# Kernel tuning notes

Hardware: AMD Instinct MI355X
Metric: run time of the kernel (lower is better)

## Reference

```python
import jax, jax.numpy as jnp
import numpy as np

CHANNELS = 32


def _mlp(x, W1, b1, W2, b2, W3, b3):
    # FNN: Linear -> ReLU -> Linear -> ReLU -> Linear (last layer linear)
    h = jax.nn.relu(x @ W1 + b1)
    h = jax.nn.relu(h @ W2 + b2)
    return h @ W3 + b3


def setup_inputs() -> dict:
    key = jax.random.key(0)
    ks = jax.random.split(key, 8)
    E = 262144
    C = CHANNELS
    H = 128
    d_in = 4  # 2 * spatial_dim
    d_out = C * (C + 1)  # 1056
    s = lambda fan_in: 1.0 / np.sqrt(fan_in)
    return {
        "pos_i": jax.random.normal(ks[0], (E, 2), jnp.float32),
        "pos_j": jax.random.normal(ks[1], (E, 2), jnp.float32),
        "v_j": jax.random.normal(ks[2], (E, C), jnp.float32),
        "W1": jax.random.normal(ks[3], (d_in, H), jnp.float32) * s(d_in),
        "b1": jnp.zeros((H,), jnp.float32),
        "W2": jax.random.normal(ks[4], (H, H), jnp.float32) * s(H),
        "b2": jnp.zeros((H,), jnp.float32),
        "W3": jax.random.normal(ks[5], (H, d_out), jnp.float32) * s(H),
        "b3": jnp.zeros((d_out,), jnp.float32),
    }


def reference(pos_i, pos_j, v_j, W1, b1, W2, b2, W3, b3):
    C = CHANNELS
    pos_ij = jnp.concatenate((pos_i, pos_j), axis=-1)          # [E, 2*spatial_dim]
    kernel = _mlp(pos_ij, W1, b1, W2, b2, W3, b3)
    kernel = kernel.reshape(-1, C, C + 1)                      # [E, C, C+1]
    mat, bias = kernel[..., :, :-1], kernel[..., :, -1]        # [E,C,C], [E,C]
    return jnp.einsum('eij,ej->ei', mat, v_j) + bias           # [E, C]
```

## Files before the change

kernel.cpp:

```cpp
#include <hip/hip_runtime.h>


#define E_TOTAL 262144
#define EPB 256
#define NBLK (E_TOTAL / EPB)

typedef float f32x4 __attribute__((ext_vector_type(4)));
typedef short s8v  __attribute__((ext_vector_type(8)));

__device__ __forceinline__ unsigned short f2bf(float x) {
  unsigned u = __float_as_uint(x);
  u += 0x7fffu + ((u >> 16) & 1u);
  return (unsigned short)(u >> 16);
}

__global__ void prep_pack(const float* __restrict__ W2, const float* __restrict__ W3,
                          const float* __restrict__ b3,
                          unsigned short* __restrict__ Wg2, unsigned short* __restrict__ W2f,
                          unsigned short* __restrict__ b3f, float* __restrict__ b3c) {
  int idx = blockIdx.x * 256 + threadIdx.x;
  if (idx < 135168) {
    int jj = idx & 7, lane = (idx >> 3) & 63;
    int ksnn = idx >> 9, ks = ksnn & 3, nn = ksnn >> 2;
    int nnt = (nn < 33) ? (2 * nn) : (2 * (nn - 33) + 1);
    int k = ks * 32 + ((lane >> 4) << 3) + jj;
    int col = nnt * 16 + (lane & 15);
    int i = col & 31, j = col >> 5;
    Wg2[idx] = f2bf(W3[k * 1056 + i * 33 + j]);
  }
  if (idx < 16384) {
    int ks = idx >> 12, nt = (idx >> 9) & 7, l = (idx >> 3) & 63, jj = idx & 7;
    int k = ks * 32 + ((l >> 4) << 3) + jj;
    int n = nt * 16 + (l & 15);
    W2f[idx] = f2bf(W2[k * 128 + n]);
  }
  if (idx < 1024) {
    int jj = idx & 7, lane = (idx >> 3) & 63, ih = idx >> 9;
    int j = ((lane >> 4) << 3) + jj, i = ih * 16 + (lane & 15);
    b3f[idx] = f2bf(b3[i * 33 + j]);
  }
  if (idx < 32) b3c[idx] = b3[idx * 33 + 32];
}

__device__ __forceinline__ void tile_load(s8v (&dst)[4], const unsigned short* __restrict__ Wg2,
                                          int n, int lane) {
  const s8v* src = (const s8v*)(Wg2 + (size_t)n * 2048 + lane * 8);
#pragma unroll
  for (int ks = 0; ks < 4; ++ks) dst[ks] = src[ks * 64];
}

template <int IH>
__device__ __forceinline__ void tile_compute(const s8v (&bf)[4], const float* __restrict__ vt,
                                             int j, int eoff,
                                             const s8v (&af)[4][4], float (&oa)[2][4][4]) {
  const f32x4 zero4 = {0.f, 0.f, 0.f, 0.f};
  const float* vp = vt + j * 260 + eoff;
#pragma unroll
  for (int m = 0; m < 4; ++m) {
    f32x4 p = __builtin_amdgcn_mfma_f32_16x16x32_bf16(af[m][0], bf[0], zero4, 0, 0, 0);
#pragma unroll
    for (int ks = 1; ks < 4; ++ks)
      p = __builtin_amdgcn_mfma_f32_16x16x32_bf16(af[m][ks], bf[ks], p, 0, 0, 0);
    f32x4 vv = *(const f32x4*)(vp + m * 16);
#pragma unroll
    for (int r = 0; r < 4; ++r) oa[IH][m][r] += vv[r] * p[r];
  }
}

__global__ __launch_bounds__(256, 2) void fnn_fused(
    const float* __restrict__ pos_i, const float* __restrict__ pos_j,
    const float* __restrict__ vj, const float* __restrict__ W1,
    const float* __restrict__ b1, const float* __restrict__ b2,
    const unsigned short* __restrict__ W2f, const unsigned short* __restrict__ Wg2,
    const unsigned short* __restrict__ b3f, const float* __restrict__ b3c,
    float* __restrict__ out) {
  __shared__ __attribute__((aligned(16))) char smem[34320];
  float* vt = (float*)smem;
  unsigned short* h2n = (unsigned short*)smem;
  unsigned short* h1c = (unsigned short*)(smem + 17408);

  const int tid = threadIdx.x;
  const int w = tid >> 6, lane = tid & 63, q = lane >> 4, ln = lane & 15;
  const int B0 = blockIdx.x * EPB;
  const int eoff = w * 64 + q * 4;

  float oa[2][4][4];
  {
    s8v av[4];
#pragma unroll
    for (int m = 0; m < 4; ++m) {
      int e = B0 + w * 64 + m * 16 + ln;
      const float4 va = *(const float4*)(vj + (size_t)e * 32 + q * 8);
      const float4 vb = *(const float4*)(vj + (size_t)e * 32 + q * 8 + 4);
      s8v t;
      t[0] = (short)f2bf(va.x); t[1] = (short)f2bf(va.y);
      t[2] = (short)f2bf(va.z); t[3] = (short)f2bf(va.w);
      t[4] = (short)f2bf(vb.x); t[5] = (short)f2bf(vb.y);
      t[6] = (short)f2bf(vb.z); t[7] = (short)f2bf(vb.w);
      av[m] = t;
    }
#pragma unroll
    for (int ih = 0; ih < 2; ++ih) {
      s8v b3fr = *(const s8v*)(b3f + (ih * 64 + lane) * 8);
      float cbv = b3c[ih * 16 + ln];
      f32x4 ci = {cbv, cbv, cbv, cbv};
#pragma unroll
      for (int m = 0; m < 4; ++m) {
        f32x4 p = __builtin_amdgcn_mfma_f32_16x16x32_bf16(av[m], b3fr, ci, 0, 0, 0);
#pragma unroll
        for (int r = 0; r < 4; ++r) oa[ih][m][r] = p[r];
      }
    }
  }

  const int hh0 = (tid & 15) * 8;
  float w1r[4][8], b1r[8];
#pragma unroll
  for (int d = 0; d < 4; ++d)
#pragma unroll
    for (int u = 0; u < 8; ++u) w1r[d][u] = W1[d * 128 + hh0 + u];
#pragma unroll
  for (int u = 0; u < 8; ++u) b1r[u] = b1[hh0 + u];

  s8v af[4][4];
  for (int qtr = 0; qtr < 4; ++qtr) {
    for (int cb = 0; cb < 2; ++cb) {
#pragma unroll
      for (int half = 0; half < 2; ++half) {
        int ee = (tid >> 4) + half * 16;
        int eg = B0 + qtr * 64 + cb * 32 + ee;
        float2 pi = *(const float2*)(pos_i + (size_t)eg * 2);
        float2 pj = *(const float2*)(pos_j + (size_t)eg * 2);
        s8v hv;
#pragma unroll
        for (int u = 0; u < 8; ++u) {
          float o = b1r[u] + pi.x * w1r[0][u] + pi.y * w1r[1][u] +
                    pj.x * w1r[2][u] + pj.y * w1r[3][u];
          hv[u] = (short)f2bf(fmaxf(o, 0.f));
        }
        *(s8v*)&h1c[ee * 136 + hh0] = hv;
      }
      __syncthreads();
#pragma unroll
      for (int s = 0; s < 4; ++s) {
        int tt = w * 4 + s, mt = tt >> 3, nt = tt & 7;
        f32x4 a4 = {0.f, 0.f, 0.f, 0.f};
#pragma unroll
        for (int ks = 0; ks < 4; ++ks) {
          s8v afr = *(const s8v*)&h1c[(mt * 16 + ln) * 136 + ks * 32 + q * 8];
          s8v bfr = *(const s8v*)(W2f + ((ks * 8 + nt) * 64 + lane) * 8);
          a4 = __builtin_amdgcn_mfma_f32_16x16x32_bf16(afr, bfr, a4, 0, 0, 0);
        }
        float b2v = b2[nt * 16 + ln];
        int eb = cb * 32 + mt * 16 + q * 4;
        int kc = nt * 16 + ln;
#pragma unroll
        for (int r = 0; r < 4; ++r)
          h2n[(eb + r) * 136 + kc] = f2bf(fmaxf(a4[r] + b2v, 0.f));
      }
      __syncthreads();
    }
    if (w == qtr) {
#pragma unroll
      for (int m = 0; m < 4; ++m)
#pragma unroll
        for (int ks = 0; ks < 4; ++ks)
          af[m][ks] = *(const s8v*)&h2n[(m * 16 + ln) * 136 + ks * 32 + q * 8];
    }
    __syncthreads();
  }

  s8v bf[4];
  tile_load(bf, Wg2, 0, lane);

  {
    const float* vrow = vj + (size_t)(B0 + tid) * 32;
#pragma unroll
    for (int j4 = 0; j4 < 8; ++j4) {
      float4 vv = *(const float4*)(vrow + j4 * 4);
      vt[(j4 * 4 + 0) * 260 + tid] = vv.x;
      vt[(j4 * 4 + 1) * 260 + tid] = vv.y;
      vt[(j4 * 4 + 2) * 260 + tid] = vv.z;
      vt[(j4 * 4 + 3) * 260 + tid] = vv.w;
    }
    vt[32 * 260 + tid] = 1.0f;
  }

#pragma unroll 1
  for (int n = 0; n < 33; ++n) {
    tile_compute<0>(bf, vt, n, eoff, af, oa);
    tile_load(bf, Wg2, n + 1, lane);
  }
#pragma unroll 1
  for (int n = 33; n < 66; ++n) {
    tile_compute<1>(bf, vt, n - 33, eoff, af, oa);
    tile_load(bf, Wg2, n + 1, lane);
  }

#pragma unroll
  for (int m = 0; m < 4; ++m)
#pragma unroll
    for (int ih = 0; ih < 2; ++ih)
#pragma unroll
      for (int r = 0; r < 4; ++r) {
        int e = B0 + w * 64 + m * 16 + q * 4 + r;
        out[(size_t)e * 32 + ih * 16 + ln] = oa[ih][m][r];
      }
}

extern "C" void kernel_launch(void* const* d_in, const int* in_sizes, int n_in,
                              void* d_out, int out_size, void* d_ws, size_t ws_size,
                              hipStream_t stream) {
  const float* pos_i = (const float*)d_in[0];
  const float* pos_j = (const float*)d_in[1];
  const float* vj    = (const float*)d_in[2];
  const float* W1    = (const float*)d_in[3];
  const float* b1    = (const float*)d_in[4];
  const float* W2    = (const float*)d_in[5];
  const float* b2    = (const float*)d_in[6];
  const float* W3    = (const float*)d_in[7];
  const float* b3    = (const float*)d_in[8];
  float* outp = (float*)d_out;

  unsigned short* Wg2 = (unsigned short*)d_ws;
  unsigned short* W2f = (unsigned short*)((char*)d_ws + 270336);
  unsigned short* b3f = (unsigned short*)((char*)d_ws + 303104);
  float*          b3c = (float*)((char*)d_ws + 305152);

  prep_pack<<<528, 256, 0, stream>>>(W2, W3, b3, Wg2, W2f, b3f, b3c);
  fnn_fused<<<NBLK, 256, 0, stream>>>(pos_i, pos_j, vj, W1, b1, b2, W2f, Wg2, b3f, b3c, outp);
}
```

Before: 184.8 us.

## Double-buffer W3 tile loads and split output halves to cut accumulator registers

The W3 tile loop now uses two register buffers so each global load has a full tile of compute to hide behind, instead of being consumed right after issue. The accumulator array shrinks from two output halves to one: the first half is stored and the second half re-initialised from v_j and the b3 bias between the two loops. This frees registers for the extra buffer, at the cost of re-reading v_j and earlier-issued stores. The v_j load for the FMA is also moved ahead of the MFMA chain.

```diff
diff --git a/kernel.cpp b/kernel.cpp
--- a/kernel.cpp
+++ b/kernel.cpp
@@ -49,22 +49,55 @@
   for (int ks = 0; ks < 4; ++ks) dst[ks] = src[ks * 64];
 }
 
-template <int IH>
 __device__ __forceinline__ void tile_compute(const s8v (&bf)[4], const float* __restrict__ vt,
                                              int j, int eoff,
-                                             const s8v (&af)[4][4], float (&oa)[2][4][4]) {
+                                             const s8v (&af)[4][4], float (&oa)[4][4]) {
   const f32x4 zero4 = {0.f, 0.f, 0.f, 0.f};
   const float* vp = vt + j * 260 + eoff;
 #pragma unroll
   for (int m = 0; m < 4; ++m) {
+    f32x4 vv = *(const f32x4*)(vp + m * 16);
     f32x4 p = __builtin_amdgcn_mfma_f32_16x16x32_bf16(af[m][0], bf[0], zero4, 0, 0, 0);
 #pragma unroll
     for (int ks = 1; ks < 4; ++ks)
       p = __builtin_amdgcn_mfma_f32_16x16x32_bf16(af[m][ks], bf[ks], p, 0, 0, 0);
-    f32x4 vv = *(const f32x4*)(vp + m * 16);
-#pragma unroll
-    for (int r = 0; r < 4; ++r) oa[IH][m][r] += vv[r] * p[r];
-  }
+#pragma unroll
+    for (int r = 0; r < 4; ++r) oa[m][r] += vv[r] * p[r];
+  }
+}
+
+__device__ __forceinline__ void init_oa(float (&oa)[4][4], const float* __restrict__ vj,
+                                        const unsigned short* __restrict__ b3f,
+                                        const float* __restrict__ b3c,
+                                        int B0, int w, int q, int ln, int lane, int ih) {
+  s8v b3fr = *(const s8v*)(b3f + (ih * 64 + lane) * 8);
+  float cbv = b3c[ih * 16 + ln];
+  f32x4 ci = {cbv, cbv, cbv, cbv};
+#pragma unroll
+  for (int m = 0; m < 4; ++m) {
+    int e = B0 + w * 64 + m * 16 + ln;
+    const float4 va = *(const float4*)(vj + (size_t)e * 32 + q * 8);
+    const float4 vb = *(const float4*)(vj + (size_t)e * 32 + q * 8 + 4);
+    s8v t;
+    t[0] = (short)f2bf(va.x); t[1] = (short)f2bf(va.y);
+    t[2] = (short)f2bf(va.z); t[3] = (short)f2bf(va.w);
+    t[4] = (short)f2bf(vb.x); t[5] = (short)f2bf(vb.y);
+    t[6] = (short)f2bf(vb.z); t[7] = (short)f2bf(vb.w);
+    f32x4 p = __builtin_amdgcn_mfma_f32_16x16x32_bf16(t, b3fr, ci, 0, 0, 0);
+#pragma unroll
+    for (int r = 0; r < 4; ++r) oa[m][r] = p[r];
+  }
+}
+
+__device__ __forceinline__ void store_half(float* __restrict__ out, const float (&oa)[4][4],
+                                           int B0, int w, int q, int ln, int ih) {
+#pragma unroll
+  for (int m = 0; m < 4; ++m)
+#pragma unroll
+    for (int r = 0; r < 4; ++r) {
+      int e = B0 + w * 64 + m * 16 + q * 4 + r;
+      out[(size_t)e * 32 + ih * 16 + ln] = oa[m][r];
+    }
 }
 
 __global__ __launch_bounds__(256, 2) void fnn_fused(
@@ -84,34 +117,8 @@
   const int B0 = blockIdx.x * EPB;
   const int eoff = w * 64 + q * 4;
 
-  float oa[2][4][4];
-  {
-    s8v av[4];
-#pragma unroll
-    for (int m = 0; m < 4; ++m) {
-      int e = B0 + w * 64 + m * 16 + ln;
-      const float4 va = *(const float4*)(vj + (size_t)e * 32 + q * 8);
-      const float4 vb = *(const float4*)(vj + (size_t)e * 32 + q * 8 + 4);
-      s8v t;
-      t[0] = (short)f2bf(va.x); t[1] = (short)f2bf(va.y);
-      t[2] = (short)f2bf(va.z); t[3] = (short)f2bf(va.w);
-      t[4] = (short)f2bf(vb.x); t[5] = (short)f2bf(vb.y);
-      t[6] = (short)f2bf(vb.z); t[7] = (short)f2bf(vb.w);
-      av[m] = t;
-    }
-#pragma unroll
-    for (int ih = 0; ih < 2; ++ih) {
-      s8v b3fr = *(const s8v*)(b3f + (ih * 64 + lane) * 8);
-      float cbv = b3c[ih * 16 + ln];
-      f32x4 ci = {cbv, cbv, cbv, cbv};
-#pragma unroll
-      for (int m = 0; m < 4; ++m) {
-        f32x4 p = __builtin_amdgcn_mfma_f32_16x16x32_bf16(av[m], b3fr, ci, 0, 0, 0);
-#pragma unroll
-        for (int r = 0; r < 4; ++r) oa[ih][m][r] = p[r];
-      }
-    }
-  }
+  float oa[4][4];
+  init_oa(oa, vj, b3f, b3c, B0, w, q, ln, lane, 0);
 
   const int hh0 = (tid & 15) * 8;
   float w1r[4][8], b1r[8];
@@ -170,8 +177,9 @@
     __syncthreads();
   }
 
-  s8v bf[4];
-  tile_load(bf, Wg2, 0, lane);
+  s8v bfA[4], bfB[4];
+  tile_load(bfA, Wg2, 0, lane);
+  tile_load(bfB, Wg2, 1, lane);
 
   {
     const float* vrow = vj + (size_t)(B0 + tid) * 32;
@@ -187,25 +195,27 @@
   }
 
 #pragma unroll 1
-  for (int n = 0; n < 33; ++n) {
-    tile_compute<0>(bf, vt, n, eoff, af, oa);
-    tile_load(bf, Wg2, n + 1, lane);
-  }
+  for (int c = 0; c < 16; ++c) {
+    tile_compute(bfA, vt, 2 * c,     eoff, af, oa);
+    tile_load(bfA, Wg2, 2 * c + 2, lane);
+    tile_compute(bfB, vt, 2 * c + 1, eoff, af, oa);
+    tile_load(bfB, Wg2, 2 * c + 3, lane);
+  }
+  tile_compute(bfA, vt, 32, eoff, af, oa);
+  tile_load(bfA, Wg2, 34, lane);
+
+  store_half(out, oa, B0, w, q, ln, 0);
+  init_oa(oa, vj, b3f, b3c, B0, w, q, ln, lane, 1);
+
 #pragma unroll 1
-  for (int n = 33; n < 66; ++n) {
-    tile_compute<1>(bf, vt, n - 33, eoff, af, oa);
-    tile_load(bf, Wg2, n + 1, lane);
-  }
-
-#pragma unroll
-  for (int m = 0; m < 4; ++m)
-#pragma unroll
-    for (int ih = 0; ih < 2; ++ih)
-#pragma unroll
-      for (int r = 0; r < 4; ++r) {
-        int e = B0 + w * 64 + m * 16 + q * 4 + r;
-        out[(size_t)e * 32 + ih * 16 + ln] = oa[ih][m][r];
-      }
+  for (int c = 0; c < 16; ++c) {
+    tile_compute(bfB, vt, 2 * c,     eoff, af, oa);
+    tile_load(bfB, Wg2, 35 + 2 * c, lane);
+    tile_compute(bfA, vt, 2 * c + 1, eoff, af, oa);
+    tile_load(bfA, Wg2, 36 + 2 * c, lane);
+  }
+  tile_compute(bfB, vt, 32, eoff, af, oa);
+  store_half(out, oa, B0, w, q, ln, 1);
 }
 
 extern "C" void kernel_launch(void* const* d_in, const int* in_sizes, int n_in,
```

New measurement: 184.9 us. Within noise of the previous version (+0.1%).

## Stage W2 fragments in LDS and restructure layer-2 into 64-edge chunks

Applied to the files above, without the earlier changes.

Copies the packed W2 bf16 fragments into shared memory with direct global-to-LDS loads at kernel start, so layer-2 MFMA operands are read from LDS instead of global memory on every chunk. Layer 2 now handles 64 edges per step, each wave computing 16 rows across all 8 column tiles. This halves the barriers per quarter and removes one, and b2 is hoisted into registers. The prep kernel is rewritten to read W3/W2 coalesced and scatter writes. LDS use roughly doubles to about 66KB, which may limit occupancy to two blocks per CU and must still fit with launch bounds.

```diff
diff --git a/kernel.cpp b/kernel.cpp
--- a/kernel.cpp
+++ b/kernel.cpp
@@ -7,11 +7,17 @@
 
 typedef float f32x4 __attribute__((ext_vector_type(4)));
 typedef short s8v  __attribute__((ext_vector_type(8)));
+typedef unsigned int u32;
 
 __device__ __forceinline__ unsigned short f2bf(float x) {
   unsigned u = __float_as_uint(x);
   u += 0x7fffu + ((u >> 16) & 1u);
   return (unsigned short)(u >> 16);
+}
+
+__device__ __forceinline__ void ld16_g2l(const void* g, void* l) {
+  __builtin_amdgcn_global_load_lds((const __attribute__((address_space(1))) u32*)g,
+                                   (__attribute__((address_space(3))) u32*)l, 16, 0, 0);
 }
 
 __global__ void prep_pack(const float* __restrict__ W2, const float* __restrict__ W3,
@@ -20,19 +26,23 @@
                           unsigned short* __restrict__ b3f, float* __restrict__ b3c) {
   int idx = blockIdx.x * 256 + threadIdx.x;
   if (idx < 135168) {
-    int jj = idx & 7, lane = (idx >> 3) & 63;
-    int ksnn = idx >> 9, ks = ksnn & 3, nn = ksnn >> 2;
-    int nnt = (nn < 33) ? (2 * nn) : (2 * (nn - 33) + 1);
-    int k = ks * 32 + ((lane >> 4) << 3) + jj;
-    int col = nnt * 16 + (lane & 15);
-    int i = col & 31, j = col >> 5;
-    Wg2[idx] = f2bf(W3[k * 1056 + i * 33 + j]);
+    int k = idx / 1056, c = idx % 1056;
+    int i = c / 33, jc = c % 33;
+    int col = jc * 32 + i;
+    int nnt = col >> 4, low = col & 15;
+    int nn = (nnt & 1) ? (33 + (nnt >> 1)) : (nnt >> 1);
+    int ks = k >> 5, kr = k & 31;
+    int lane = ((kr >> 3) << 4) + low;
+    int jj = k & 7;
+    Wg2[((nn * 4 + ks) * 64 + lane) * 8 + jj] = f2bf(W3[idx]);
   }
   if (idx < 16384) {
-    int ks = idx >> 12, nt = (idx >> 9) & 7, l = (idx >> 3) & 63, jj = idx & 7;
-    int k = ks * 32 + ((l >> 4) << 3) + jj;
-    int n = nt * 16 + (l & 15);
-    W2f[idx] = f2bf(W2[k * 128 + n]);
+    int k = idx >> 7, n = idx & 127;
+    int ks = k >> 5, kr = k & 31;
+    int nt = n >> 4, low = n & 15;
+    int l = ((kr >> 3) << 4) + low;
+    int jj = k & 7;
+    W2f[((ks * 8 + nt) * 64 + l) * 8 + jj] = f2bf(W2[idx]);
   }
   if (idx < 1024) {
     int jj = idx & 7, lane = (idx >> 3) & 63, ih = idx >> 9;
@@ -74,15 +84,24 @@
     const unsigned short* __restrict__ W2f, const unsigned short* __restrict__ Wg2,
     const unsigned short* __restrict__ b3f, const float* __restrict__ b3c,
     float* __restrict__ out) {
-  __shared__ __attribute__((aligned(16))) char smem[34320];
+  __shared__ __attribute__((aligned(16))) char smem[67584];
   float* vt = (float*)smem;
-  unsigned short* h2n = (unsigned short*)smem;
-  unsigned short* h1c = (unsigned short*)(smem + 17408);
+  unsigned short* h1c = (unsigned short*)smem;
+  unsigned short* h2n = (unsigned short*)(smem + 17408);
+  unsigned short* W2L = (unsigned short*)(smem + 34816);
 
   const int tid = threadIdx.x;
   const int w = tid >> 6, lane = tid & 63, q = lane >> 4, ln = lane & 15;
   const int B0 = blockIdx.x * EPB;
   const int eoff = w * 64 + q * 4;
+
+  {
+    const unsigned short* src = W2f + tid * 8;
+    char* dstb = smem + 34816 + w * 1024;
+#pragma unroll
+    for (int cc = 0; cc < 8; ++cc)
+      ld16_g2l(src + cc * 2048, dstb + cc * 4096);
+  }
 
   float oa[2][4][4];
   {
@@ -114,52 +133,52 @@
   }
 
   const int hh0 = (tid & 15) * 8;
-  float w1r[4][8], b1r[8];
+  float w1r[4][8], b1r[8], b2r[8];
 #pragma unroll
   for (int d = 0; d < 4; ++d)
 #pragma unroll
     for (int u = 0; u < 8; ++u) w1r[d][u] = W1[d * 128 + hh0 + u];
 #pragma unroll
   for (int u = 0; u < 8; ++u) b1r[u] = b1[hh0 + u];
+#pragma unroll
+  for (int s = 0; s < 8; ++s) b2r[s] = b2[s * 16 + ln];
 
   s8v af[4][4];
   for (int qtr = 0; qtr < 4; ++qtr) {
-    for (int cb = 0; cb < 2; ++cb) {
-#pragma unroll
-      for (int half = 0; half < 2; ++half) {
-        int ee = (tid >> 4) + half * 16;
-        int eg = B0 + qtr * 64 + cb * 32 + ee;
-        float2 pi = *(const float2*)(pos_i + (size_t)eg * 2);
-        float2 pj = *(const float2*)(pos_j + (size_t)eg * 2);
-        s8v hv;
-#pragma unroll
-        for (int u = 0; u < 8; ++u) {
-          float o = b1r[u] + pi.x * w1r[0][u] + pi.y * w1r[1][u] +
-                    pj.x * w1r[2][u] + pj.y * w1r[3][u];
-          hv[u] = (short)f2bf(fmaxf(o, 0.f));
-        }
-        *(s8v*)&h1c[ee * 136 + hh0] = hv;
-      }
-      __syncthreads();
-#pragma unroll
-      for (int s = 0; s < 4; ++s) {
-        int tt = w * 4 + s, mt = tt >> 3, nt = tt & 7;
-        f32x4 a4 = {0.f, 0.f, 0.f, 0.f};
-#pragma unroll
-        for (int ks = 0; ks < 4; ++ks) {
-          s8v afr = *(const s8v*)&h1c[(mt * 16 + ln) * 136 + ks * 32 + q * 8];
-          s8v bfr = *(const s8v*)(W2f + ((ks * 8 + nt) * 64 + lane) * 8);
-          a4 = __builtin_amdgcn_mfma_f32_16x16x32_bf16(afr, bfr, a4, 0, 0, 0);
-        }
-        float b2v = b2[nt * 16 + ln];
-        int eb = cb * 32 + mt * 16 + q * 4;
-        int kc = nt * 16 + ln;
-#pragma unroll
-        for (int r = 0; r < 4; ++r)
-          h2n[(eb + r) * 136 + kc] = f2bf(fmaxf(a4[r] + b2v, 0.f));
-      }
-      __syncthreads();
-    }
+#pragma unroll
+    for (int half = 0; half < 4; ++half) {
+      int ee = (tid >> 4) + half * 16;
+      int eg = B0 + qtr * 64 + ee;
+      float2 pi = *(const float2*)(pos_i + (size_t)eg * 2);
+      float2 pj = *(const float2*)(pos_j + (size_t)eg * 2);
+      s8v hv;
+#pragma unroll
+      for (int u = 0; u < 8; ++u) {
+        float o = b1r[u] + pi.x * w1r[0][u] + pi.y * w1r[1][u] +
+                  pj.x * w1r[2][u] + pj.y * w1r[3][u];
+        hv[u] = (short)f2bf(fmaxf(o, 0.f));
+      }
+      *(s8v*)&h1c[ee * 136 + hh0] = hv;
+    }
+    __syncthreads();
+
+#pragma unroll
+    for (int s = 0; s < 8; ++s) {
+      f32x4 a4 = {0.f, 0.f, 0.f, 0.f};
+#pragma unroll
+      for (int ks = 0; ks < 4; ++ks) {
+        s8v afr = *(const s8v*)&h1c[(w * 16 + ln) * 136 + ks * 32 + q * 8];
+        s8v bfr = *(const s8v*)&W2L[((ks * 8 + s) * 64 + lane) * 8];
+        a4 = __builtin_amdgcn_mfma_f32_16x16x32_bf16(afr, bfr, a4, 0, 0, 0);
+      }
+      int eb = w * 16 + q * 4;
+      int kc = s * 16 + ln;
+#pragma unroll
+      for (int r = 0; r < 4; ++r)
+        h2n[(eb + r) * 136 + kc] = f2bf(fmaxf(a4[r] + b2r[s], 0.f));
+    }
+    __syncthreads();
+
     if (w == qtr) {
 #pragma unroll
       for (int m = 0; m < 4; ++m)
@@ -167,8 +186,8 @@
         for (int ks = 0; ks < 4; ++ks)
           af[m][ks] = *(const s8v*)&h2n[(m * 16 + ln) * 136 + ks * 32 + q * 8];
     }
-    __syncthreads();
-  }
+  }
+  __syncthreads();
 
   s8v bf[4];
   tile_load(bf, Wg2, 0, lane);
```

Result: faster. 176.6 us, median of 2 (-4.4%).
